# Optimization experiments

Measured on AMD Instinct MI355X. Metric: run time of the kernel, lower is better.

Reference implementation:

```python
import jax, jax.numpy as jnp
import numpy as np

H = 8          # nheads
D_OUT = 1024   # tf_out_dim
D_HEAD = D_OUT // H
LN_EPS = 1e-5


def setup_inputs() -> dict:
    key = jax.random.key(0)
    ks = jax.random.split(key, 8)
    n_tok, d_in = 512, 1024
    return {
        "x": jax.random.normal(ks[0], (n_tok, d_in), jnp.float32),
        "c": jax.random.normal(ks[1], (H, n_tok, D_HEAD, D_HEAD), jnp.float32),
        "m_prev": jax.random.normal(ks[2], (H, n_tok, 1), jnp.float32),
        "n_prev": jax.random.normal(ks[3], (H, n_tok, D_HEAD), jnp.float32),
        "Wqkvo": jax.random.normal(ks[4], (d_in, 4 * D_OUT), jnp.float32) * 0.02,
        "bqkvo": jax.random.normal(ks[5], (4 * D_OUT,), jnp.float32) * 0.02,
        "Wuf": jax.random.normal(ks[6], (d_in, 2 * H), jnp.float32) * 0.02,
        "buf": jax.random.normal(ks[7], (2 * H,), jnp.float32) * 0.02,
    }


def reference(x, c, m_prev, n_prev, Wqkvo, bqkvo, Wuf, buf):
    n_tok = x.shape[0]
    scale = jnp.sqrt(jnp.float32(D_HEAD))  # sqrt(tf_out_dim / nheads)

    # projections: 'n (h d) -> h n d'
    qkvo = (x @ Wqkvo + bqkvo).reshape(n_tok, H, 4 * D_HEAD).transpose(1, 0, 2)
    q, k, v, o = jnp.split(qkvo, 4, axis=-1)          # each (H, n, d)
    k = k / scale

    # per-token outer-product update matrix ct = v k^T : (H, n, d, d)
    ct = v[..., :, None] * k[..., None, :]

    uf = (x @ Wuf + buf).reshape(n_tok, H, 2).transpose(1, 0, 2)  # (H, n, 2)
    u, f = uf[..., 0:1], uf[..., 1:2]                  # (H, n, 1)

    # stabilized exp gating (gate='exp', c is not None branch)
    m = jnp.maximum(f + m_prev, u)                     # (H, n, 1)
    ue = jnp.exp(u - m)
    fe = jnp.exp(f + m_prev - m)

    c_new = fe[..., None] * c + ue[..., None] * ct     # (H, n, d, d)
    n_new = fe * n_prev + ue * k                       # (H, n, d)

    # readout (note: original uses ct, not c_new, in the readout einsum)
    h = jnp.einsum('hnkl,hnl->hnk', ct, q)             # (H, n, d)
    nm = jnp.abs(jnp.einsum('hnk,hnk->hn', n_new, q))  # (H, n)
    h = h / jnp.maximum(nm, 1.0)[..., None]
    h = h * jax.nn.sigmoid(o)

    # 'h n d -> n (h d)', residual, LayerNorm over last dim (no affine)
    h = h.transpose(1, 0, 2).reshape(n_tok, D_OUT)
    h = x + h
    mu = jnp.mean(h, axis=-1, keepdims=True)
    var = jnp.var(h, axis=-1, keepdims=True)
    h = (h - mu) / jnp.sqrt(var + LN_EPS)
    return (c_new, h)
```

## Files before the change

kernel.cpp:

```cpp
#include <hip/hip_runtime.h>
#include <hip/hip_bf16.h>
#include <math.h>

#define KSCALE 0.08838834764831845f

typedef __bf16 bf16x8 __attribute__((ext_vector_type(8)));
typedef float  f32x4  __attribute__((ext_vector_type(4)));
typedef unsigned short u16x4 __attribute__((ext_vector_type(4)));
typedef unsigned short u16x8 __attribute__((ext_vector_type(8)));

__device__ inline unsigned short f2bf(float f) {
    unsigned int u = __float_as_uint(f);
    unsigned int r = (u + 0x7FFFu + ((u >> 16) & 1u)) >> 16;
    return (unsigned short)r;
}

__global__ __launch_bounds__(256) void prep_kernel(const float* __restrict__ x,
                                                   unsigned short* __restrict__ xb,
                                                   const float* __restrict__ W,
                                                   unsigned short* __restrict__ Wt) {
    int b = blockIdx.x;
    if (b < 512) {
        int t = b * 256 + threadIdx.x;
        float4 v = reinterpret_cast<const float4*>(x)[t];
        u16x4 o = { f2bf(v.x), f2bf(v.y), f2bf(v.z), f2bf(v.w) };
        reinterpret_cast<u16x4*>(xb)[t] = o;
    } else {
        __shared__ float tile[32][33];
        int bb = b - 512;
        int bk = bb & 31;
        int bn = bb >> 5;
        int k0 = bk * 32, n0 = bn * 32;
        int r = threadIdx.x >> 5, col = threadIdx.x & 31;
#pragma unroll
        for (int it = 0; it < 4; ++it)
            tile[r + it * 8][col] = W[(size_t)(k0 + r + it * 8) * 4096 + n0 + col];
        __syncthreads();
#pragma unroll
        for (int it = 0; it < 4; ++it)
            Wt[(size_t)(n0 + r + it * 8) * 1024 + k0 + col] = f2bf(tile[col][r + it * 8]);
    }
}

__global__ __launch_bounds__(256) void gemm_qkvo(const unsigned short* __restrict__ A,
                                                 const unsigned short* __restrict__ Bt,
                                                 const float* __restrict__ bias,
                                                 float* __restrict__ C) {
    __shared__ __align__(16) unsigned short As[64][72];
    __shared__ __align__(16) unsigned short Bs[64][72];
    const int bm = blockIdx.x & 7;
    const int bn = blockIdx.x >> 3;
    const int m0 = bm * 64, n0 = bn * 64;
    const int tid = threadIdx.x;
    const int lane = tid & 63, wave = tid >> 6;
    const int wr = wave >> 1, wc = wave & 1;
    f32x4 acc[2][2] = {};

    for (int k0 = 0; k0 < 1024; k0 += 64) {
#pragma unroll
        for (int c = 0; c < 2; ++c) {
            int chunk = tid + c * 256;
            int r = chunk >> 3, col = (chunk & 7) * 8;
            *reinterpret_cast<u16x8*>(&As[r][col]) =
                *reinterpret_cast<const u16x8*>(&A[(size_t)(m0 + r) * 1024 + k0 + col]);
            *reinterpret_cast<u16x8*>(&Bs[r][col]) =
                *reinterpret_cast<const u16x8*>(&Bt[(size_t)(n0 + r) * 1024 + k0 + col]);
        }
        __syncthreads();
        const int row = lane & 15;
        const int kof = (lane >> 4) * 8;
#pragma unroll
        for (int kk = 0; kk < 2; ++kk) {
            int kb = kk * 32 + kof;
            bf16x8 a0 = *reinterpret_cast<const bf16x8*>(&As[wr * 32 + row][kb]);
            bf16x8 a1 = *reinterpret_cast<const bf16x8*>(&As[wr * 32 + 16 + row][kb]);
            bf16x8 b0 = *reinterpret_cast<const bf16x8*>(&Bs[wc * 32 + row][kb]);
            bf16x8 b1 = *reinterpret_cast<const bf16x8*>(&Bs[wc * 32 + 16 + row][kb]);
            acc[0][0] = __builtin_amdgcn_mfma_f32_16x16x32_bf16(a0, b0, acc[0][0], 0, 0, 0);
            acc[0][1] = __builtin_amdgcn_mfma_f32_16x16x32_bf16(a0, b1, acc[0][1], 0, 0, 0);
            acc[1][0] = __builtin_amdgcn_mfma_f32_16x16x32_bf16(a1, b0, acc[1][0], 0, 0, 0);
            acc[1][1] = __builtin_amdgcn_mfma_f32_16x16x32_bf16(a1, b1, acc[1][1], 0, 0, 0);
        }
        __syncthreads();
    }
    const int cn = lane & 15, cm = (lane >> 4) * 4;
#pragma unroll
    for (int i = 0; i < 2; ++i)
#pragma unroll
        for (int j = 0; j < 2; ++j) {
            int gm = m0 + wr * 32 + i * 16 + cm;
            int gn = n0 + wc * 32 + j * 16 + cn;
            float b = bias[gn];
#pragma unroll
            for (int v = 0; v < 4; ++v)
                C[(size_t)(gm + v) * 4096 + gn] = acc[i][j][v] + b;
        }
}

__global__ __launch_bounds__(256) void uf_gates(const float* __restrict__ x,
                                                const float* __restrict__ Wuf,
                                                const float* __restrict__ buf,
                                                const float* __restrict__ m_prev,
                                                float* __restrict__ fe_ue) {
    const int n = blockIdx.x;
    const int tid = threadIdx.x;
    const int lane = tid & 63, w = tid >> 6;
    const float* xr = x + (size_t)n * 1024;
    float4 p = {0.f, 0.f, 0.f, 0.f};
#pragma unroll
    for (int i = 0; i < 16; ++i) {
        int k = lane + i * 64;
        float xv = xr[k];
        float4 wv = *reinterpret_cast<const float4*>(&Wuf[(size_t)k * 16 + 4 * w]);
        p.x += xv * wv.x; p.y += xv * wv.y; p.z += xv * wv.z; p.w += xv * wv.w;
    }
#pragma unroll
    for (int off = 32; off; off >>= 1) {
        p.x += __shfl_down(p.x, off);
        p.y += __shfl_down(p.y, off);
        p.z += __shfl_down(p.z, off);
        p.w += __shfl_down(p.w, off);
    }
    if (lane == 0) {
#pragma unroll
        for (int t = 0; t < 2; ++t) {
            int h = 2 * w + t;
            float u = (t ? p.z : p.x) + buf[4 * w + 2 * t];
            float f = (t ? p.w : p.y) + buf[4 * w + 2 * t + 1];
            float mp = m_prev[h * 512 + n];
            float m = fmaxf(f + mp, u);
            fe_ue[(h * 512 + n) * 2 + 0] = expf(f + mp - m);
            fe_ue[(h * 512 + n) * 2 + 1] = expf(u - m);
        }
    }
}

__global__ __launch_bounds__(256) void fuse_main(const float* __restrict__ qkvo,
                                                 const float* __restrict__ c_in,
                                                 const float* __restrict__ n_prev,
                                                 const float* __restrict__ fe_ue,
                                                 float* __restrict__ c_out,
                                                 float* __restrict__ hst) {
    const int blk = blockIdx.x;
    const int h = blk >> 9, n = blk & 511;
    const int tid = threadIdx.x;
    __shared__ float k_s[128], v_s[128];
    __shared__ float rkq[4], rnq[4];

    const float* base = qkvo + (size_t)n * 4096 + h * 512;
    const float fe = fe_ue[(h * 512 + n) * 2 + 0];
    const float ue = fe_ue[(h * 512 + n) * 2 + 1];

    float kq_p = 0.f, nq_p = 0.f;
    if (tid < 128) {
        float q = base[tid];
        float k = base[128 + tid] * KSCALE;
        float v = base[256 + tid];
        k_s[tid] = k;
        v_s[tid] = v;
        float nn = fe * n_prev[(size_t)(h * 512 + n) * 128 + tid] + ue * k;
        kq_p = k * q;
        nq_p = nn * q;
    }
#pragma unroll
    for (int off = 32; off; off >>= 1) {
        kq_p += __shfl_down(kq_p, off);
        nq_p += __shfl_down(nq_p, off);
    }
    if ((tid & 63) == 0) { rkq[tid >> 6] = kq_p; rnq[tid >> 6] = nq_p; }
    __syncthreads();
    const float kq = rkq[0] + rkq[1];
    const float nm = fabsf(rnq[0] + rnq[1]);
    const float g = kq / fmaxf(nm, 1.0f);

    const f32x4* cin4 = reinterpret_cast<const f32x4*>(c_in + (size_t)(h * 512 + n) * 16384);
    f32x4* cout4 = reinterpret_cast<f32x4*>(c_out + (size_t)(h * 512 + n) * 16384);
#pragma unroll
    for (int it = 0; it < 16; ++it) {
        int e4 = tid + it * 256;
        int i = e4 >> 5;
        int j4 = (e4 & 31) * 4;
        f32x4 cv = __builtin_nontemporal_load(&cin4[e4]);
        float uv = ue * v_s[i];
        f32x4 o;
        o.x = fe * cv.x + uv * k_s[j4 + 0];
        o.y = fe * cv.y + uv * k_s[j4 + 1];
        o.z = fe * cv.z + uv * k_s[j4 + 2];
        o.w = fe * cv.w + uv * k_s[j4 + 3];
        __builtin_nontemporal_store(o, &cout4[e4]);
    }

    if (tid < 128) {
        float o = base[384 + tid];
        float sig = 1.f / (1.f + expf(-o));
        hst[(size_t)n * 1024 + h * 128 + tid] = v_s[tid] * g * sig;
    }
}

__global__ __launch_bounds__(256) void ln_kernel(const float* __restrict__ x,
                                                 const float* __restrict__ hst,
                                                 float* __restrict__ out) {
    int n = blockIdx.x, tid = threadIdx.x;
    float4 hv = reinterpret_cast<const float4*>(hst + (size_t)n * 1024)[tid];
    float4 xv = reinterpret_cast<const float4*>(x + (size_t)n * 1024)[tid];
    float4 s = { hv.x + xv.x, hv.y + xv.y, hv.z + xv.z, hv.w + xv.w };
    float sum = s.x + s.y + s.z + s.w;
    float sq = s.x * s.x + s.y * s.y + s.z * s.z + s.w * s.w;
#pragma unroll
    for (int off = 32; off; off >>= 1) {
        sum += __shfl_down(sum, off);
        sq += __shfl_down(sq, off);
    }
    __shared__ float rs[4], rq[4];
    if ((tid & 63) == 0) { rs[tid >> 6] = sum; rq[tid >> 6] = sq; }
    __syncthreads();
    sum = rs[0] + rs[1] + rs[2] + rs[3];
    sq = rq[0] + rq[1] + rq[2] + rq[3];
    float mu = sum * (1.f / 1024.f);
    float var = sq * (1.f / 1024.f) - mu * mu;
    float inv = rsqrtf(var + 1e-5f);
    float4 o4 = { (s.x - mu) * inv, (s.y - mu) * inv, (s.z - mu) * inv, (s.w - mu) * inv };
    reinterpret_cast<float4*>(out)[(size_t)n * 256 + tid] = o4;
}

extern "C" void kernel_launch(void* const* d_in, const int* in_sizes, int n_in,
                              void* d_out, int out_size, void* d_ws, size_t ws_size,
                              hipStream_t stream) {
    const float* x      = (const float*)d_in[0];
    const float* c_in   = (const float*)d_in[1];
    const float* m_prev = (const float*)d_in[2];
    const float* n_prev = (const float*)d_in[3];
    const float* Wqkvo  = (const float*)d_in[4];
    const float* bqkvo  = (const float*)d_in[5];
    const float* Wuf    = (const float*)d_in[6];
    const float* buf    = (const float*)d_in[7];
    float* out = (float*)d_out;
    char* ws = (char*)d_ws;

    unsigned short* xb   = (unsigned short*)(ws);
    unsigned short* Wt   = (unsigned short*)(ws + (1u << 20));
    float* qkvo          = (float*)(ws + 9u * (1u << 20));
    float* fe_ue         = (float*)(ws + 17u * (1u << 20));
    float* hst           = (float*)(ws + 17u * (1u << 20) + (1u << 16));

    prep_kernel<<<dim3(4608), dim3(256), 0, stream>>>(x, xb, Wqkvo, Wt);
    uf_gates   <<<dim3(512),  dim3(256), 0, stream>>>(x, Wuf, buf, m_prev, fe_ue);
    gemm_qkvo  <<<dim3(512),  dim3(256), 0, stream>>>(xb, Wt, bqkvo, qkvo);
    fuse_main  <<<dim3(4096), dim3(256), 0, stream>>>(qkvo, c_in, n_prev, fe_ue, out, hst);
    ln_kernel  <<<dim3(512),  dim3(256), 0, stream>>>(x, hst, out + 67108864ull);
}
```

Baseline: 142.4 us.

## Double-buffer GEMM with direct-to-LDS loads and fold gate kernel into prep

The QKVO GEMM now stages tiles through two LDS buffers filled by global_load_lds, so the next K-tile is prefetched while the current one feeds MFMA and one barrier per iteration is dropped. The separate uf_gates kernel is merged into prep_kernel as extra blocks, removing one launch. The unpadded LDS layout may add bank conflicts on fragment reads, and the overall gain is bounded because the large c tensor traffic dominates.

```diff
diff --git a/kernel.cpp b/kernel.cpp
--- a/kernel.cpp
+++ b/kernel.cpp
@@ -15,17 +15,28 @@
     return (unsigned short)r;
 }
 
+__device__ __forceinline__ void gll16(const unsigned short* g, unsigned short* l) {
+    __builtin_amdgcn_global_load_lds(
+        (const __attribute__((address_space(1))) unsigned int*)g,
+        (__attribute__((address_space(3))) unsigned int*)l,
+        16, 0, 0);
+}
+
 __global__ __launch_bounds__(256) void prep_kernel(const float* __restrict__ x,
                                                    unsigned short* __restrict__ xb,
                                                    const float* __restrict__ W,
-                                                   unsigned short* __restrict__ Wt) {
+                                                   unsigned short* __restrict__ Wt,
+                                                   const float* __restrict__ Wuf,
+                                                   const float* __restrict__ buf,
+                                                   const float* __restrict__ m_prev,
+                                                   float* __restrict__ fe_ue) {
     int b = blockIdx.x;
     if (b < 512) {
         int t = b * 256 + threadIdx.x;
         float4 v = reinterpret_cast<const float4*>(x)[t];
         u16x4 o = { f2bf(v.x), f2bf(v.y), f2bf(v.z), f2bf(v.w) };
         reinterpret_cast<u16x4*>(xb)[t] = o;
-    } else {
+    } else if (b < 4608) {
         __shared__ float tile[32][33];
         int bb = b - 512;
         int bk = bb & 31;
@@ -39,6 +50,38 @@
 #pragma unroll
         for (int it = 0; it < 4; ++it)
             Wt[(size_t)(n0 + r + it * 8) * 1024 + k0 + col] = f2bf(tile[col][r + it * 8]);
+    } else {
+        const int n = b - 4608;
+        const int tid = threadIdx.x;
+        const int lane = tid & 63, w = tid >> 6;
+        const float* xr = x + (size_t)n * 1024;
+        float4 p = {0.f, 0.f, 0.f, 0.f};
+#pragma unroll
+        for (int i = 0; i < 16; ++i) {
+            int k = lane + i * 64;
+            float xv = xr[k];
+            float4 wv = *reinterpret_cast<const float4*>(&Wuf[(size_t)k * 16 + 4 * w]);
+            p.x += xv * wv.x; p.y += xv * wv.y; p.z += xv * wv.z; p.w += xv * wv.w;
+        }
+#pragma unroll
+        for (int off = 32; off; off >>= 1) {
+            p.x += __shfl_down(p.x, off);
+            p.y += __shfl_down(p.y, off);
+            p.z += __shfl_down(p.z, off);
+            p.w += __shfl_down(p.w, off);
+        }
+        if (lane == 0) {
+#pragma unroll
+            for (int t = 0; t < 2; ++t) {
+                int h = 2 * w + t;
+                float u = (t ? p.z : p.x) + buf[4 * w + 2 * t];
+                float f = (t ? p.w : p.y) + buf[4 * w + 2 * t + 1];
+                float mp = m_prev[h * 512 + n];
+                float m = fmaxf(f + mp, u);
+                fe_ue[(h * 512 + n) * 2 + 0] = expf(f + mp - m);
+                fe_ue[(h * 512 + n) * 2 + 1] = expf(u - m);
+            }
+        }
     }
 }
 
@@ -46,8 +89,8 @@
                                                  const unsigned short* __restrict__ Bt,
                                                  const float* __restrict__ bias,
                                                  float* __restrict__ C) {
-    __shared__ __align__(16) unsigned short As[64][72];
-    __shared__ __align__(16) unsigned short Bs[64][72];
+    __shared__ __align__(16) unsigned short As[2][64 * 64];
+    __shared__ __align__(16) unsigned short Bs[2][64 * 64];
     const int bm = blockIdx.x & 7;
     const int bn = blockIdx.x >> 3;
     const int m0 = bm * 64, n0 = bn * 64;
@@ -56,33 +99,50 @@
     const int wr = wave >> 1, wc = wave & 1;
     f32x4 acc[2][2] = {};
 
-    for (int k0 = 0; k0 < 1024; k0 += 64) {
-#pragma unroll
-        for (int c = 0; c < 2; ++c) {
-            int chunk = tid + c * 256;
-            int r = chunk >> 3, col = (chunk & 7) * 8;
-            *reinterpret_cast<u16x8*>(&As[r][col]) =
-                *reinterpret_cast<const u16x8*>(&A[(size_t)(m0 + r) * 1024 + k0 + col]);
-            *reinterpret_cast<u16x8*>(&Bs[r][col]) =
-                *reinterpret_cast<const u16x8*>(&Bt[(size_t)(n0 + r) * 1024 + k0 + col]);
-        }
-        __syncthreads();
+    const int srow = lane >> 3;
+    const int scol = (lane & 7) * 8;
+
+#pragma unroll
+    for (int c = 0; c < 2; ++c) {
+        int chunk = wave * 2 + c;
+        int row = chunk * 8 + srow;
+        gll16(A + (size_t)(m0 + row) * 1024 + scol, &As[0][chunk * 512]);
+        gll16(Bt + (size_t)(n0 + row) * 1024 + scol, &Bs[0][chunk * 512]);
+    }
+    __syncthreads();
+
+    int cur = 0;
+    for (int t = 0; t < 16; ++t) {
+        if (t < 15) {
+            int k0 = (t + 1) * 64;
+#pragma unroll
+            for (int c = 0; c < 2; ++c) {
+                int chunk = wave * 2 + c;
+                int row = chunk * 8 + srow;
+                gll16(A + (size_t)(m0 + row) * 1024 + k0 + scol, &As[cur ^ 1][chunk * 512]);
+                gll16(Bt + (size_t)(n0 + row) * 1024 + k0 + scol, &Bs[cur ^ 1][chunk * 512]);
+            }
+        }
+        const unsigned short* as = As[cur];
+        const unsigned short* bs = Bs[cur];
         const int row = lane & 15;
         const int kof = (lane >> 4) * 8;
 #pragma unroll
         for (int kk = 0; kk < 2; ++kk) {
             int kb = kk * 32 + kof;
-            bf16x8 a0 = *reinterpret_cast<const bf16x8*>(&As[wr * 32 + row][kb]);
-            bf16x8 a1 = *reinterpret_cast<const bf16x8*>(&As[wr * 32 + 16 + row][kb]);
-            bf16x8 b0 = *reinterpret_cast<const bf16x8*>(&Bs[wc * 32 + row][kb]);
-            bf16x8 b1 = *reinterpret_cast<const bf16x8*>(&Bs[wc * 32 + 16 + row][kb]);
+            bf16x8 a0 = *reinterpret_cast<const bf16x8*>(&as[(wr * 32 + row) * 64 + kb]);
+            bf16x8 a1 = *reinterpret_cast<const bf16x8*>(&as[(wr * 32 + 16 + row) * 64 + kb]);
+            bf16x8 b0 = *reinterpret_cast<const bf16x8*>(&bs[(wc * 32 + row) * 64 + kb]);
+            bf16x8 b1 = *reinterpret_cast<const bf16x8*>(&bs[(wc * 32 + 16 + row) * 64 + kb]);
             acc[0][0] = __builtin_amdgcn_mfma_f32_16x16x32_bf16(a0, b0, acc[0][0], 0, 0, 0);
             acc[0][1] = __builtin_amdgcn_mfma_f32_16x16x32_bf16(a0, b1, acc[0][1], 0, 0, 0);
             acc[1][0] = __builtin_amdgcn_mfma_f32_16x16x32_bf16(a1, b0, acc[1][0], 0, 0, 0);
             acc[1][1] = __builtin_amdgcn_mfma_f32_16x16x32_bf16(a1, b1, acc[1][1], 0, 0, 0);
         }
         __syncthreads();
-    }
+        cur ^= 1;
+    }
+
     const int cn = lane & 15, cm = (lane >> 4) * 4;
 #pragma unroll
     for (int i = 0; i < 2; ++i)
@@ -95,44 +155,6 @@
             for (int v = 0; v < 4; ++v)
                 C[(size_t)(gm + v) * 4096 + gn] = acc[i][j][v] + b;
         }
-}
-
-__global__ __launch_bounds__(256) void uf_gates(const float* __restrict__ x,
-                                                const float* __restrict__ Wuf,
-                                                const float* __restrict__ buf,
-                                                const float* __restrict__ m_prev,
-                                                float* __restrict__ fe_ue) {
-    const int n = blockIdx.x;
-    const int tid = threadIdx.x;
-    const int lane = tid & 63, w = tid >> 6;
-    const float* xr = x + (size_t)n * 1024;
-    float4 p = {0.f, 0.f, 0.f, 0.f};
-#pragma unroll
-    for (int i = 0; i < 16; ++i) {
-        int k = lane + i * 64;
-        float xv = xr[k];
-        float4 wv = *reinterpret_cast<const float4*>(&Wuf[(size_t)k * 16 + 4 * w]);
-        p.x += xv * wv.x; p.y += xv * wv.y; p.z += xv * wv.z; p.w += xv * wv.w;
-    }
-#pragma unroll
-    for (int off = 32; off; off >>= 1) {
-        p.x += __shfl_down(p.x, off);
-        p.y += __shfl_down(p.y, off);
-        p.z += __shfl_down(p.z, off);
-        p.w += __shfl_down(p.w, off);
-    }
-    if (lane == 0) {
-#pragma unroll
-        for (int t = 0; t < 2; ++t) {
-            int h = 2 * w + t;
-            float u = (t ? p.z : p.x) + buf[4 * w + 2 * t];
-            float f = (t ? p.w : p.y) + buf[4 * w + 2 * t + 1];
-            float mp = m_prev[h * 512 + n];
-            float m = fmaxf(f + mp, u);
-            fe_ue[(h * 512 + n) * 2 + 0] = expf(f + mp - m);
-            fe_ue[(h * 512 + n) * 2 + 1] = expf(u - m);
-        }
-    }
 }
 
 __global__ __launch_bounds__(256) void fuse_main(const float* __restrict__ qkvo,
@@ -243,8 +265,7 @@
     float* fe_ue         = (float*)(ws + 17u * (1u << 20));
     float* hst           = (float*)(ws + 17u * (1u << 20) + (1u << 16));
 
-    prep_kernel<<<dim3(4608), dim3(256), 0, stream>>>(x, xb, Wqkvo, Wt);
-    uf_gates   <<<dim3(512),  dim3(256), 0, stream>>>(x, Wuf, buf, m_prev, fe_ue);
+    prep_kernel<<<dim3(5120), dim3(256), 0, stream>>>(x, xb, Wqkvo, Wt, Wuf, buf, m_prev, fe_ue);
     gemm_qkvo  <<<dim3(512),  dim3(256), 0, stream>>>(xb, Wt, bqkvo, qkvo);
     fuse_main  <<<dim3(4096), dim3(256), 0, stream>>>(qkvo, c_in, n_prev, fe_ue, out, hst);
     ln_kernel  <<<dim3(512),  dim3(256), 0, stream>>>(x, hst, out + 67108864ull);
```

After: 136.6 us. 1.04x faster.
